# Performance work log

Measured on AMD Instinct MI355X. Metric: run time of the kernel, lower is better.

Reference implementation:

```python
import jax, jax.numpy as jnp
import numpy as np

N = 131072        # total nodes in batched graph
E = 2097152       # total edges (avg degree 16)
F_IN = 256        # input feature dim
DIMS = [64, 32, 16]
G = 128           # number of graphs in batch


def setup_inputs() -> dict:
    key = jax.random.key(0)
    ks = jax.random.split(key, 16)
    inp = {
        "features": jax.random.normal(ks[0], (N, F_IN), jnp.float32),
        "src": jax.random.randint(ks[1], (E,), 0, N),
        "dst": jax.random.randint(ks[2], (E,), 0, N),
        "graph_ids": jnp.sort(jax.random.randint(ks[3], (N,), 0, G)),
    }
    d = F_IN
    for i, out in enumerate(DIMS):
        inp[f"W{i}"] = jax.random.normal(ks[4 + 2 * i], (d, out), jnp.float32) / np.sqrt(d).astype(np.float32)
        inp[f"b{i}"] = jax.random.normal(ks[5 + 2 * i], (out,), jnp.float32) * 0.01
        d = out
    inp["Wc"] = jax.random.normal(ks[10], (DIMS[-1], 1), jnp.float32) / np.sqrt(DIMS[-1]).astype(np.float32)
    inp["bc"] = jax.random.normal(ks[11], (1,), jnp.float32) * 0.01
    return inp


def _graph_conv(h, W, b, src, dst, src_norm, dst_norm):
    # DGL GraphConv, norm='both', activation=relu, allow_zero_in_degree=True
    # (in_feats > out_feats everywhere here, so project before aggregating)
    hw = (h * src_norm) @ W                       # [N, out]
    agg = jax.ops.segment_sum(hw[src], dst, num_segments=N)  # gather->scatter-add
    return jax.nn.relu(agg * dst_norm + b)


def reference(features, src, dst, graph_ids, W0, b0, W1, b1, W2, b2, Wc, bc):
    ones_e = jnp.ones((E,), jnp.float32)
    out_deg = jax.ops.segment_sum(ones_e, src, num_segments=N)
    in_deg = jax.ops.segment_sum(ones_e, dst, num_segments=N)
    # DGL clamps degrees to >=1 before pow(-0.5)
    src_norm = jnp.power(jnp.maximum(out_deg, 1.0), -0.5)[:, None]  # [N,1]
    dst_norm = jnp.power(jnp.maximum(in_deg, 1.0), -0.5)[:, None]

    h = features
    for W, b in ((W0, b0), (W1, b1), (W2, b2)):
        h = _graph_conv(h, W, b, src, dst, src_norm, dst_norm)

    # dgl.mean_nodes over batched graph
    sums = jax.ops.segment_sum(h, graph_ids, num_segments=G)          # [G,16]
    cnt = jax.ops.segment_sum(jnp.ones((N,), jnp.float32), graph_ids, num_segments=G)
    hg = sums / jnp.maximum(cnt, 1.0)[:, None]

    return (hg @ Wc + bc).squeeze(-1)  # [G] logits
```

## Files before the change

### kernel.cpp

```cpp
#include <hip/hip_runtime.h>

#define N_NODES 131072
#define N_EDGES 2097152
#define N_GRAPHS 128
#define POOL_NPB 256
#define NB 256
#define BUCKET_SHIFT 9
#define BUCKET_CAP 9728
#define BIN_EPT 32

__global__ __launch_bounds__(256) void k_init_buckets(int* __restrict__ cursor_d,
                                                      int* __restrict__ cursor_s) {
  int i = threadIdx.x;
  cursor_d[i] = i * BUCKET_CAP;
  cursor_s[i] = i * BUCKET_CAP;
}

__global__ __launch_bounds__(256) void k_bin(const int* __restrict__ src,
                                             const int* __restrict__ dst,
                                             int* __restrict__ cursor_d,
                                             int* __restrict__ cursor_s,
                                             unsigned int* __restrict__ recs_d,
                                             unsigned short* __restrict__ recs_s) {
  __shared__ int hd[NB];
  __shared__ int hs[NB];
  const int t = threadIdx.x;
  const int e0 = blockIdx.x * (256 * BIN_EPT);
  hd[t] = 0; hs[t] = 0;
  __syncthreads();
#pragma unroll 4
  for (int k = 0; k < BIN_EPT; ++k) {
    int e = e0 + k * 256 + t;
    atomicAdd(&hd[dst[e] >> BUCKET_SHIFT], 1);
    atomicAdd(&hs[src[e] >> BUCKET_SHIFT], 1);
  }
  __syncthreads();
  { int c = hd[t]; hd[t] = c ? atomicAdd(&cursor_d[t], c) : 0; }
  { int c = hs[t]; hs[t] = c ? atomicAdd(&cursor_s[t], c) : 0; }
  __syncthreads();
#pragma unroll 4
  for (int k = 0; k < BIN_EPT; ++k) {
    int e = e0 + k * 256 + t;
    int s = src[e];
    int d = dst[e];
    int pd = atomicAdd(&hd[d >> BUCKET_SHIFT], 1);
    recs_d[pd] = ((unsigned int)s << BUCKET_SHIFT) | (unsigned int)(d & 511);
    int ps = atomicAdd(&hs[s >> BUCKET_SHIFT], 1);
    recs_s[ps] = (unsigned short)(s & 511);
  }
}

__global__ __launch_bounds__(512) void k_outdeg(const unsigned short* __restrict__ recs_s,
                                                const int* __restrict__ cursor_s,
                                                float* __restrict__ src_norm) {
  __shared__ int hist[512];
  const int b = blockIdx.x;
  const int t = threadIdx.x;
  hist[t] = 0;
  __syncthreads();
  const int beg = b * BUCKET_CAP;
  const int end = cursor_s[b];
  for (int i = beg + t; i < end; i += 512) atomicAdd(&hist[recs_s[i]], 1);
  __syncthreads();
  int od = hist[t]; if (od < 1) od = 1;
  src_norm[b * 512 + t] = 1.0f / sqrtf((float)od);
}

__global__ __launch_bounds__(256) void k_bucket_scan(const int* __restrict__ cursor_d,
                                                     int* __restrict__ bucket_base,
                                                     int* __restrict__ row_start) {
  __shared__ int tmp[256];
  int t = threadIdx.x;
  int c = cursor_d[t] - t * BUCKET_CAP;
  tmp[t] = c;
  __syncthreads();
  for (int off = 1; off < 256; off <<= 1) {
    int x = (t >= off) ? tmp[t - off] : 0;
    __syncthreads();
    tmp[t] += x;
    __syncthreads();
  }
  bucket_base[t] = tmp[t] - c;
  if (t == 0) row_start[N_NODES] = N_EDGES;
}

__global__ __launch_bounds__(512) void k_fill2(const unsigned int* __restrict__ recs_d,
                                               const int* __restrict__ cursor_d,
                                               const int* __restrict__ bucket_base,
                                               int* __restrict__ row_start,
                                               float* __restrict__ dst_norm,
                                               int* __restrict__ csr_src) {
  __shared__ int hist[512];
  __shared__ int lcur[512];
  const int b = blockIdx.x;
  const int t = threadIdx.x;
  hist[t] = 0;
  __syncthreads();
  const int beg = b * BUCKET_CAP;
  const int end = cursor_d[b];
  for (int i = beg + t; i < end; i += 512) atomicAdd(&hist[recs_d[i] & 511], 1);
  __syncthreads();
  int deg = hist[t];
  lcur[t] = deg;
  __syncthreads();
  for (int off = 1; off < 512; off <<= 1) {
    int x = (t >= off) ? lcur[t - off] : 0;
    __syncthreads();
    lcur[t] += x;
    __syncthreads();
  }
  int rs = bucket_base[b] + lcur[t] - deg;
  row_start[b * 512 + t] = rs;
  int dd = deg < 1 ? 1 : deg;
  dst_norm[b * 512 + t] = 1.0f / sqrtf((float)dd);
  lcur[t] = rs;
  __syncthreads();
  for (int i = beg + t; i < end; i += 512) {
    unsigned int r = recs_d[i];
    int p = atomicAdd(&lcur[r & 511], 1);
    csr_src[p] = (int)(r >> BUCKET_SHIFT);
  }
}

template <int DIN, int DOUT>
__global__ __launch_bounds__(256) void k_gemm(const float* __restrict__ h,
                                              const float* __restrict__ src_norm,
                                              const float* __restrict__ W,
                                              float* __restrict__ out) {
  constexpr int KC   = 32;
  constexpr int ROWS = 64;
  constexpr int NCH  = DIN / KC;
  constexpr int CPW  = DOUT / 4;
  __shared__ float hT[KC][ROWS];

  const int t    = threadIdx.x;
  const int lane = t & 63;
  const int wv   = __builtin_amdgcn_readfirstlane(t >> 6);
  const int rowBase = blockIdx.x * ROWS;
  const int rg0 = t >> 3;
  const int ks  = (t & 7) * 4;

  float acc[CPW];
#pragma unroll
  for (int j = 0; j < CPW; ++j) acc[j] = 0.0f;

  for (int ch = 0; ch < NCH; ++ch) {
    const int kc = ch * KC;
#pragma unroll
    for (int p = 0; p < 2; ++p) {
      int rg = rg0 + 32 * p;
      float4 v = *reinterpret_cast<const float4*>(&h[(size_t)(rowBase + rg) * DIN + kc + ks]);
      hT[ks + 0][rg ^ ((((ks + 0) >> 3) & 3) << 3)] = v.x;
      hT[ks + 1][rg ^ ((((ks + 1) >> 3) & 3) << 3)] = v.y;
      hT[ks + 2][rg ^ ((((ks + 2) >> 3) & 3) << 3)] = v.z;
      hT[ks + 3][rg ^ ((((ks + 3) >> 3) & 3) << 3)] = v.w;
    }
    __syncthreads();
    const float* Wrow = &W[(size_t)kc * DOUT + wv * CPW];
#pragma unroll
    for (int kk = 0; kk < KC; ++kk) {
      const int swz = ((kk >> 3) & 3) << 3;
      float a = hT[kk][lane ^ swz];
#pragma unroll
      for (int j = 0; j < CPW; ++j)
        acc[j] += a * Wrow[kk * DOUT + j];
    }
    __syncthreads();
  }

  const int row = rowBase + lane;
  float nrm = src_norm[row];
  float* op = &out[(size_t)row * DOUT + wv * CPW];
#pragma unroll
  for (int q = 0; q < CPW / 4; ++q) {
    float4 v = {acc[q * 4 + 0] * nrm, acc[q * 4 + 1] * nrm,
                acc[q * 4 + 2] * nrm, acc[q * 4 + 3] * nrm};
    *reinterpret_cast<float4*>(op + q * 4) = v;
  }
}

template <int D>
__global__ __launch_bounds__(256) void k_agg(const float* __restrict__ hw,
                                             const int* __restrict__ row_start,
                                             const int* __restrict__ csr_src,
                                             const float* __restrict__ dst_norm,
                                             const float* __restrict__ bias,
                                             float* __restrict__ out) {
  constexpr int LPN = D / 4;
  constexpr int NPW = 64 / LPN;
  const int t = threadIdx.x;
  const int lane = t & 63;
  const int wave = t >> 6;
  const int f4  = (lane % LPN) * 4;
  const int sub = lane / LPN;
  const int node = (blockIdx.x * 4 + wave) * NPW + sub;
  const int start = row_start[node];
  const int end   = row_start[node + 1];
  float ax = 0.0f, ay = 0.0f, az = 0.0f, aw = 0.0f;
  int i = start;
  for (; i + 4 <= end; i += 4) {
    int s0 = csr_src[i + 0];
    int s1 = csr_src[i + 1];
    int s2 = csr_src[i + 2];
    int s3 = csr_src[i + 3];
    float4 v0 = *reinterpret_cast<const float4*>(&hw[(size_t)s0 * D + f4]);
    float4 v1 = *reinterpret_cast<const float4*>(&hw[(size_t)s1 * D + f4]);
    float4 v2 = *reinterpret_cast<const float4*>(&hw[(size_t)s2 * D + f4]);
    float4 v3 = *reinterpret_cast<const float4*>(&hw[(size_t)s3 * D + f4]);
    ax += v0.x + v1.x + v2.x + v3.x;
    ay += v0.y + v1.y + v2.y + v3.y;
    az += v0.z + v1.z + v2.z + v3.z;
    aw += v0.w + v1.w + v2.w + v3.w;
  }
  for (; i < end; ++i) {
    float4 v = *reinterpret_cast<const float4*>(&hw[(size_t)csr_src[i] * D + f4]);
    ax += v.x; ay += v.y; az += v.z; aw += v.w;
  }
  float nrm = dst_norm[node];
  float4 b4 = *reinterpret_cast<const float4*>(&bias[f4]);
  float4 r;
  r.x = fmaxf(ax * nrm + b4.x, 0.0f);
  r.y = fmaxf(ay * nrm + b4.y, 0.0f);
  r.z = fmaxf(az * nrm + b4.z, 0.0f);
  r.w = fmaxf(aw * nrm + b4.w, 0.0f);
  *reinterpret_cast<float4*>(&out[(size_t)node * D + f4]) = r;
}

__global__ __launch_bounds__(256) void k_pool(const float* __restrict__ h3,
                                              const int* __restrict__ gid,
                                              float* __restrict__ sums,
                                              float* __restrict__ cnt) {
  const int t = threadIdx.x;
  const int f = t & 15;
  const int grp = t >> 4;
  const int base = blockIdx.x * POOL_NPB;
  float acc = 0.0f, c = 0.0f;
  int cur = gid[base + grp];
#pragma unroll 4
  for (int k = 0; k < POOL_NPB / 16; ++k) {
    int node = base + grp + k * 16;
    int g = gid[node];
    float v = h3[(size_t)node * 16 + f];
    if (g != cur) {
      atomicAdd(&sums[cur * 16 + f], acc);
      if (f == 0) atomicAdd(&cnt[cur], c);
      acc = 0.0f; c = 0.0f; cur = g;
    }
    acc += v; c += 1.0f;
  }
  atomicAdd(&sums[cur * 16 + f], acc);
  if (f == 0) atomicAdd(&cnt[cur], c);
}

__global__ __launch_bounds__(128) void k_classify(const float* __restrict__ sums,
                                                  const float* __restrict__ cnt,
                                                  const float* __restrict__ Wc,
                                                  const float* __restrict__ bc,
                                                  float* __restrict__ out) {
  int g = threadIdx.x;
  float c = cnt[g]; if (c < 1.0f) c = 1.0f;
  float acc = 0.0f;
#pragma unroll
  for (int f = 0; f < 16; ++f) acc += (sums[g * 16 + f] / c) * Wc[f];
  out[g] = acc + bc[0];
}

extern "C" void kernel_launch(void* const* d_in, const int* in_sizes, int n_in,
                              void* d_out, int out_size, void* d_ws, size_t ws_size,
                              hipStream_t stream) {
  const float* features = (const float*)d_in[0];
  const int*   src      = (const int*)d_in[1];
  const int*   dst      = (const int*)d_in[2];
  const int*   gid      = (const int*)d_in[3];
  const float* W0 = (const float*)d_in[4];
  const float* b0 = (const float*)d_in[5];
  const float* W1 = (const float*)d_in[6];
  const float* b1 = (const float*)d_in[7];
  const float* W2 = (const float*)d_in[8];
  const float* b2 = (const float*)d_in[9];
  const float* Wc = (const float*)d_in[10];
  const float* bc = (const float*)d_in[11];
  float* out = (float*)d_out;

  char* w = (char*)d_ws;
  auto alloc = [&](size_t bytes) {
    void* p = (void*)w;
    w += (bytes + 255) & ~(size_t)255;
    return p;
  };
  float* src_norm    = (float*)alloc((size_t)N_NODES * 4);
  float* dst_norm    = (float*)alloc((size_t)N_NODES * 4);
  int*   row_start   = (int*)alloc((size_t)(N_NODES + 1) * 4);
  int*   cursor_d    = (int*)alloc(NB * 4);
  int*   cursor_s    = (int*)alloc(NB * 4);
  int*   bucket_base = (int*)alloc(NB * 4);
  int*   csr_src     = (int*)alloc((size_t)N_EDGES * 4);
  float* buf0        = (float*)alloc((size_t)N_NODES * 64 * 4);
  float* buf1        = (float*)alloc((size_t)N_NODES * 64 * 4);
  float* sums        = (float*)alloc((size_t)N_GRAPHS * 16 * 4);
  float* cnt         = (float*)alloc((size_t)N_GRAPHS * 4);
  unsigned int*   recs_d = (unsigned int*)buf0;
  unsigned short* recs_s = (unsigned short*)buf1;

  hipMemsetAsync(sums, 0, (size_t)(N_GRAPHS * 16 + N_GRAPHS) * 4, stream);

  k_init_buckets<<<1, 256, 0, stream>>>(cursor_d, cursor_s);
  k_bin<<<N_EDGES / (256 * BIN_EPT), 256, 0, stream>>>(src, dst, cursor_d, cursor_s,
                                                       recs_d, recs_s);
  k_outdeg<<<NB, 512, 0, stream>>>(recs_s, cursor_s, src_norm);
  k_bucket_scan<<<1, 256, 0, stream>>>(cursor_d, bucket_base, row_start);
  k_fill2<<<NB, 512, 0, stream>>>(recs_d, cursor_d, bucket_base, row_start,
                                  dst_norm, csr_src);

  k_gemm<256, 64><<<N_NODES / 64, 256, 0, stream>>>(features, src_norm, W0, buf0);
  k_agg<64><<<N_NODES / 16, 256, 0, stream>>>(buf0, row_start, csr_src, dst_norm, b0, buf1);
  k_gemm<64, 32><<<N_NODES / 64, 256, 0, stream>>>(buf1, src_norm, W1, buf0);
  k_agg<32><<<N_NODES / 32, 256, 0, stream>>>(buf0, row_start, csr_src, dst_norm, b1, buf1);
  k_gemm<32, 16><<<N_NODES / 64, 256, 0, stream>>>(buf1, src_norm, W2, buf0);
  k_agg<16><<<N_NODES / 64, 256, 0, stream>>>(buf0, row_start, csr_src, dst_norm, b2, buf1);

  k_pool<<<N_NODES / POOL_NPB, 256, 0, stream>>>(buf1, gid, sums, cnt);
  k_classify<<<1, 128, 0, stream>>>(sums, cnt, Wc, bc, out);
}
```

Measured before the change: 339.2 us.

## Store projected features in bf16 and use one-row-per-thread GEMM

The projected per-layer features are now written in bf16 instead of fp32, which halves the bytes the random-gather aggregation kernels read per edge. The aggregations still accumulate in fp32. The GEMM is also rewritten so each thread computes a full output row, reading its input row directly and reading W through uniform (broadcast) loads, with no LDS transpose and no barriers. The costs are reduced precision in the intermediate features and higher register pressure from DOUT accumulators per thread. Each thread also reads its own row non-coalesced, which for the 256-wide first layer could stress the cache.

```diff
diff --git a/kernel.cpp b/kernel.cpp
--- a/kernel.cpp
+++ b/kernel.cpp
@@ -8,6 +8,17 @@
 #define BUCKET_SHIFT 9
 #define BUCKET_CAP 9728
 #define BIN_EPT 32
+
+__device__ __forceinline__ float bf2f(unsigned short b) {
+  return __uint_as_float(((unsigned int)b) << 16);
+}
+__device__ __forceinline__ unsigned short f2bf(float f) {
+  unsigned int u = __float_as_uint(f);
+  return (unsigned short)((u + 0x7FFFu + ((u >> 16) & 1u)) >> 16);
+}
+__device__ __forceinline__ unsigned int pack2bf(float a, float b) {
+  return (unsigned int)f2bf(a) | ((unsigned int)f2bf(b) << 16);
+}
 
 __global__ __launch_bounds__(256) void k_init_buckets(int* __restrict__ cursor_d,
                                                       int* __restrict__ cursor_s) {
@@ -123,64 +134,46 @@
 }
 
 template <int DIN, int DOUT>
-__global__ __launch_bounds__(256) void k_gemm(const float* __restrict__ h,
-                                              const float* __restrict__ src_norm,
-                                              const float* __restrict__ W,
-                                              float* __restrict__ out) {
-  constexpr int KC   = 32;
-  constexpr int ROWS = 64;
-  constexpr int NCH  = DIN / KC;
-  constexpr int CPW  = DOUT / 4;
-  __shared__ float hT[KC][ROWS];
-
-  const int t    = threadIdx.x;
-  const int lane = t & 63;
-  const int wv   = __builtin_amdgcn_readfirstlane(t >> 6);
-  const int rowBase = blockIdx.x * ROWS;
-  const int rg0 = t >> 3;
-  const int ks  = (t & 7) * 4;
-
-  float acc[CPW];
-#pragma unroll
-  for (int j = 0; j < CPW; ++j) acc[j] = 0.0f;
-
-  for (int ch = 0; ch < NCH; ++ch) {
-    const int kc = ch * KC;
-#pragma unroll
-    for (int p = 0; p < 2; ++p) {
-      int rg = rg0 + 32 * p;
-      float4 v = *reinterpret_cast<const float4*>(&h[(size_t)(rowBase + rg) * DIN + kc + ks]);
-      hT[ks + 0][rg ^ ((((ks + 0) >> 3) & 3) << 3)] = v.x;
-      hT[ks + 1][rg ^ ((((ks + 1) >> 3) & 3) << 3)] = v.y;
-      hT[ks + 2][rg ^ ((((ks + 2) >> 3) & 3) << 3)] = v.z;
-      hT[ks + 3][rg ^ ((((ks + 3) >> 3) & 3) << 3)] = v.w;
+__global__ __launch_bounds__(256) void k_gemm_v10(const float* __restrict__ h,
+                                                  const float* __restrict__ src_norm,
+                                                  const float* __restrict__ W,
+                                                  unsigned short* __restrict__ out) {
+  const int row = blockIdx.x * 256 + threadIdx.x;
+  const float* hrow = &h[(size_t)row * DIN];
+
+  float acc[DOUT];
+#pragma unroll
+  for (int j = 0; j < DOUT; ++j) acc[j] = 0.0f;
+
+  for (int kc = 0; kc < DIN; kc += 16) {
+    float4 a0 = *reinterpret_cast<const float4*>(&hrow[kc + 0]);
+    float4 a1 = *reinterpret_cast<const float4*>(&hrow[kc + 4]);
+    float4 a2 = *reinterpret_cast<const float4*>(&hrow[kc + 8]);
+    float4 a3 = *reinterpret_cast<const float4*>(&hrow[kc + 12]);
+    float av[16] = {a0.x, a0.y, a0.z, a0.w, a1.x, a1.y, a1.z, a1.w,
+                    a2.x, a2.y, a2.z, a2.w, a3.x, a3.y, a3.z, a3.w};
+#pragma unroll
+    for (int kk = 0; kk < 16; ++kk) {
+      const float* Wrow = &W[(size_t)(kc + kk) * DOUT];
+#pragma unroll
+      for (int j = 0; j < DOUT; ++j) acc[j] += av[kk] * Wrow[j];
     }
-    __syncthreads();
-    const float* Wrow = &W[(size_t)kc * DOUT + wv * CPW];
-#pragma unroll
-    for (int kk = 0; kk < KC; ++kk) {
-      const int swz = ((kk >> 3) & 3) << 3;
-      float a = hT[kk][lane ^ swz];
-#pragma unroll
-      for (int j = 0; j < CPW; ++j)
-        acc[j] += a * Wrow[kk * DOUT + j];
-    }
-    __syncthreads();
-  }
-
-  const int row = rowBase + lane;
+  }
+
   float nrm = src_norm[row];
-  float* op = &out[(size_t)row * DOUT + wv * CPW];
-#pragma unroll
-  for (int q = 0; q < CPW / 4; ++q) {
-    float4 v = {acc[q * 4 + 0] * nrm, acc[q * 4 + 1] * nrm,
-                acc[q * 4 + 2] * nrm, acc[q * 4 + 3] * nrm};
-    *reinterpret_cast<float4*>(op + q * 4) = v;
+  unsigned short* op = &out[(size_t)row * DOUT];
+#pragma unroll
+  for (int q = 0; q < DOUT / 8; ++q) {
+    uint4 v = {pack2bf(acc[q * 8 + 0] * nrm, acc[q * 8 + 1] * nrm),
+               pack2bf(acc[q * 8 + 2] * nrm, acc[q * 8 + 3] * nrm),
+               pack2bf(acc[q * 8 + 4] * nrm, acc[q * 8 + 5] * nrm),
+               pack2bf(acc[q * 8 + 6] * nrm, acc[q * 8 + 7] * nrm)};
+    *reinterpret_cast<uint4*>(&op[q * 8]) = v;
   }
 }
 
 template <int D>
-__global__ __launch_bounds__(256) void k_agg(const float* __restrict__ hw,
+__global__ __launch_bounds__(256) void k_agg(const unsigned short* __restrict__ hw,
                                              const int* __restrict__ row_start,
                                              const int* __restrict__ csr_src,
                                              const float* __restrict__ dst_norm,
@@ -203,18 +196,18 @@
     int s1 = csr_src[i + 1];
     int s2 = csr_src[i + 2];
     int s3 = csr_src[i + 3];
-    float4 v0 = *reinterpret_cast<const float4*>(&hw[(size_t)s0 * D + f4]);
-    float4 v1 = *reinterpret_cast<const float4*>(&hw[(size_t)s1 * D + f4]);
-    float4 v2 = *reinterpret_cast<const float4*>(&hw[(size_t)s2 * D + f4]);
-    float4 v3 = *reinterpret_cast<const float4*>(&hw[(size_t)s3 * D + f4]);
-    ax += v0.x + v1.x + v2.x + v3.x;
-    ay += v0.y + v1.y + v2.y + v3.y;
-    az += v0.z + v1.z + v2.z + v3.z;
-    aw += v0.w + v1.w + v2.w + v3.w;
+    ushort4 v0 = *reinterpret_cast<const ushort4*>(&hw[(size_t)s0 * D + f4]);
+    ushort4 v1 = *reinterpret_cast<const ushort4*>(&hw[(size_t)s1 * D + f4]);
+    ushort4 v2 = *reinterpret_cast<const ushort4*>(&hw[(size_t)s2 * D + f4]);
+    ushort4 v3 = *reinterpret_cast<const ushort4*>(&hw[(size_t)s3 * D + f4]);
+    ax += bf2f(v0.x) + bf2f(v1.x) + bf2f(v2.x) + bf2f(v3.x);
+    ay += bf2f(v0.y) + bf2f(v1.y) + bf2f(v2.y) + bf2f(v3.y);
+    az += bf2f(v0.z) + bf2f(v1.z) + bf2f(v2.z) + bf2f(v3.z);
+    aw += bf2f(v0.w) + bf2f(v1.w) + bf2f(v2.w) + bf2f(v3.w);
   }
   for (; i < end; ++i) {
-    float4 v = *reinterpret_cast<const float4*>(&hw[(size_t)csr_src[i] * D + f4]);
-    ax += v.x; ay += v.y; az += v.z; aw += v.w;
+    ushort4 v = *reinterpret_cast<const ushort4*>(&hw[(size_t)csr_src[i] * D + f4]);
+    ax += bf2f(v.x); ay += bf2f(v.y); az += bf2f(v.z); aw += bf2f(v.w);
   }
   float nrm = dst_norm[node];
   float4 b4 = *reinterpret_cast<const float4*>(&bias[f4]);
@@ -301,6 +294,8 @@
   float* cnt         = (float*)alloc((size_t)N_GRAPHS * 4);
   unsigned int*   recs_d = (unsigned int*)buf0;
   unsigned short* recs_s = (unsigned short*)buf1;
+  unsigned short* hw_bf  = (unsigned short*)buf0;
+  float*          hbuf   = buf1;
 
   hipMemsetAsync(sums, 0, (size_t)(N_GRAPHS * 16 + N_GRAPHS) * 4, stream);
 
@@ -312,13 +307,13 @@
   k_fill2<<<NB, 512, 0, stream>>>(recs_d, cursor_d, bucket_base, row_start,
                                   dst_norm, csr_src);
 
-  k_gemm<256, 64><<<N_NODES / 64, 256, 0, stream>>>(features, src_norm, W0, buf0);
-  k_agg<64><<<N_NODES / 16, 256, 0, stream>>>(buf0, row_start, csr_src, dst_norm, b0, buf1);
-  k_gemm<64, 32><<<N_NODES / 64, 256, 0, stream>>>(buf1, src_norm, W1, buf0);
-  k_agg<32><<<N_NODES / 32, 256, 0, stream>>>(buf0, row_start, csr_src, dst_norm, b1, buf1);
-  k_gemm<32, 16><<<N_NODES / 64, 256, 0, stream>>>(buf1, src_norm, W2, buf0);
-  k_agg<16><<<N_NODES / 64, 256, 0, stream>>>(buf0, row_start, csr_src, dst_norm, b2, buf1);
-
-  k_pool<<<N_NODES / POOL_NPB, 256, 0, stream>>>(buf1, gid, sums, cnt);
+  k_gemm_v10<256, 64><<<N_NODES / 256, 256, 0, stream>>>(features, src_norm, W0, hw_bf);
+  k_agg<64><<<N_NODES / 16, 256, 0, stream>>>(hw_bf, row_start, csr_src, dst_norm, b0, hbuf);
+  k_gemm_v10<64, 32><<<N_NODES / 256, 256, 0, stream>>>(hbuf, src_norm, W1, hw_bf);
+  k_agg<32><<<N_NODES / 32, 256, 0, stream>>>(hw_bf, row_start, csr_src, dst_norm, b1, hbuf);
+  k_gemm_v10<32, 16><<<N_NODES / 256, 256, 0, stream>>>(hbuf, src_norm, W2, hw_bf);
+  k_agg<16><<<N_NODES / 64, 256, 0, stream>>>(hw_bf, row_start, csr_src, dst_norm, b2, hbuf);
+
+  k_pool<<<N_NODES / POOL_NPB, 256, 0, stream>>>(hbuf, gid, sums, cnt);
   k_classify<<<1, 128, 0, stream>>>(sums, cnt, Wc, bc, out);
 }
```

Result: slower. 382.1 us (+12.6%).
